# Kernel tuning notes

Hardware: AMD Instinct MI355X
Metric: run time of the kernel (lower is better)

## Reference

```python
import jax, jax.numpy as jnp
import numpy as np

S = 7          # grid size
C = 10         # num classes (SVHN digits)
L_COORD = 5.0
L_NOOBJ = 0.5
EPS = 1e-6     # safe-sqrt epsilon (original sqrt(clamp(x,0,1)) has inf grad at 0)


def _iou(b1, b2):
    """Vectorized translation of computeIOU. b1, b2: [..., 4] as (left, top, w, h)."""
    l1l, l1t, w1, h1 = b1[..., 0], b1[..., 1], b1[..., 2], b1[..., 3]
    l2l, l2t, w2, h2 = b2[..., 0], b2[..., 1], b2[..., 2], b2[..., 3]
    l1r, l1b = l1l + w1, l1t + h1
    l2r, l2b = l2l + w2, l2t + h2
    a1 = w1 * h1
    a2 = w2 * h2
    cont_by2 = (l2l <= l1l) & (l2t <= l1t) & (l2r >= l1r) & (l2b >= l1b)  # box2 contains box1
    cont_by1 = (l1l <= l2l) & (l1t <= l2t) & (l1r >= l2r) & (l1b >= l2b)  # box1 contains box2
    sep = (l1r <= l2l) | (l2r <= l1l) | (l1b <= l2t) | (l2b <= l1t)       # disjoint
    iw = jnp.minimum(l1r, l2r) - jnp.maximum(l1l, l2l)
    ih = jnp.minimum(l1b, l2b) - jnp.maximum(l1t, l2t)
    inter = iw * ih
    gen = inter / (a1 + a2 - inter)
    return jnp.where(cont_by2, a1 / a2,
           jnp.where(cont_by1, a2 / a1,
           jnp.where(sep, jnp.zeros_like(gen), gen)))


def setup_inputs() -> dict:
    key = jax.random.key(0)
    k1, k2, k3, k4 = jax.random.split(key, 4)
    N = 16384
    pred_tensor = jax.random.normal(k1, (N, S, S, 20), dtype=jnp.float32)
    xywh = jax.random.uniform(k2, (N, S, S, 4), dtype=jnp.float32)
    conf = (jax.random.uniform(k3, (N, S, S, 1)) < 0.15).astype(jnp.float32)  # ~7 objects/img
    cls = jax.random.randint(k4, (N, S, S, 1), 0, C).astype(jnp.float32)
    target_tensor = jnp.concatenate([xywh, conf, cls], axis=-1)
    return {"pred_tensor": pred_tensor, "target_tensor": target_tensor}


def reference(pred_tensor, target_tensor):
    N = pred_tensor.shape[0]
    conf_t = target_tensor[..., 4]                       # [N,S,S]
    coo = (conf_t > 0).astype(pred_tensor.dtype)
    noo = (conf_t == 0).astype(pred_tensor.dtype)

    # no-object confidence loss: both predicted confidences vs target conf (=0 on noo cells)
    noobj_loss = jnp.sum(noo * ((pred_tensor[..., 4] - conf_t) ** 2 +
                                (pred_tensor[..., 9] - conf_t) ** 2))

    # responsible-box selection via IoU (vectorized replacement of the python loop)
    bt = target_tensor[..., :4]                          # target box [N,S,S,4]
    bp0 = pred_tensor[..., 0:5]
    bp1 = pred_tensor[..., 5:10]
    iou0 = _iou(bp0[..., :4], bt)
    iou1 = _iou(bp1[..., :4], bt)
    pick0 = iou0 >= iou1                                 # box0 responsible when tie or higher
    max_iou = jax.lax.stop_gradient(jnp.where(pick0, iou0, iou1))  # Variable() detach in orig
    resp = jnp.where(pick0[..., None], bp0, bp1)         # responsible pred box [N,S,S,5]
    nonresp = jnp.where(pick0[..., None], bp1, bp0)

    contain_loss = jnp.sum(coo * (resp[..., 4] - max_iou) ** 2)

    xy_p = jnp.clip(resp[..., :2], 0.0, 1.0)
    xy_t = jnp.clip(bt[..., :2], 0.0, 1.0)
    wh_p = jnp.sqrt(jnp.clip(resp[..., 2:4], EPS, 1.0))
    wh_t = jnp.sqrt(jnp.clip(bt[..., 2:4], EPS, 1.0))
    loc_loss = jnp.sum(coo[..., None] * ((xy_p - xy_t) ** 2 + (wh_p - wh_t) ** 2))

    not_contain_loss = jnp.sum(coo * nonresp[..., 4] ** 2)  # target conf forced to 0

    # class cross-entropy (sum reduction) over object cells
    logits = pred_tensor[..., 10:]                       # [N,S,S,10]
    logz = jax.nn.logsumexp(logits, axis=-1)
    cls_idx = target_tensor[..., 5].astype(jnp.int32)
    picked = jnp.take_along_axis(logits, cls_idx[..., None], axis=-1)[..., 0]
    class_loss = jnp.sum(coo * (logz - picked))

    total = (L_COORD * loc_loss + 2.0 * contain_loss + not_contain_loss +
             L_NOOBJ * noobj_loss + class_loss)
    return total / N
```

## Files before the change

### kernel.cpp

```cpp
#include <hip/hip_runtime.h>
#include <hip/hip_bf16.h>


#define SBLK 256

constexpr float L_COORD = 5.0f;
constexpr float L_NOOBJ = 0.5f;
constexpr float EPS_    = 1e-6f;

__device__ __forceinline__ float iou_f(float l1l, float l1t, float w1, float h1,
                                       float l2l, float l2t, float w2, float h2) {
    float l1r = l1l + w1, l1b = l1t + h1;
    float l2r = l2l + w2, l2b = l2t + h2;
    float a1 = w1 * h1, a2 = w2 * h2;
    bool cont_by2 = (l2l <= l1l) && (l2t <= l1t) && (l2r >= l1r) && (l2b >= l1b);
    bool cont_by1 = (l1l <= l2l) && (l1t <= l2t) && (l1r >= l2r) && (l1b >= l2b);
    bool sep = (l1r <= l2l) || (l2r <= l1l) || (l1b <= l2t) || (l2b <= l1t);
    float iw = fminf(l1r, l2r) - fmaxf(l1l, l2l);
    float ih = fminf(l1b, l2b) - fmaxf(l1t, l2t);
    float inter = iw * ih;
    float gen = inter / (a1 + a2 - inter);
    float r = sep ? 0.0f : gen;
    r = cont_by1 ? (a2 / a1) : r;
    r = cont_by2 ? (a1 / a2) : r;
    return r;
}

__device__ __forceinline__ float clamp01(float x) { return fminf(fmaxf(x, 0.0f), 1.0f); }

__global__ __launch_bounds__(SBLK) void yolo_loss_kernel(
        const float* __restrict__ pred, const float* __restrict__ tgt,
        double* __restrict__ partials, int ncells) {
    int i = blockIdx.x * SBLK + threadIdx.x;
    float total = 0.0f;
    if (i < ncells) {
        const float4* p4 = reinterpret_cast<const float4*>(pred + (size_t)i * 20);
        float4 pa = p4[0];
        float4 pb = p4[1];
        float4 pc = p4[2];
        float4 pd = p4[3];
        float4 pe = p4[4];
        const float2* t2 = reinterpret_cast<const float2*>(tgt + (size_t)i * 6);
        float2 t0 = t2[0];
        float2 t1 = t2[1];
        float2 tc = t2[2];

        float conf = tc.x;
        float coo = (conf > 0.0f) ? 1.0f : 0.0f;
        float noo = (conf == 0.0f) ? 1.0f : 0.0f;

        float d0 = pb.x - conf, d1 = pc.y - conf;
        float noobj = noo * (d0 * d0 + d1 * d1);

        float b0l = pa.x, b0t = pa.y, b0w = pa.z, b0h = pa.w, b0c = pb.x;
        float b1l = pb.y, b1t = pb.z, b1w = pb.w, b1h = pc.x, b1c = pc.y;
        float btl = t0.x, btt = t0.y, btw = t1.x, bth = t1.y;

        float iou0 = iou_f(b0l, b0t, b0w, b0h, btl, btt, btw, bth);
        float iou1 = iou_f(b1l, b1t, b1w, b1h, btl, btt, btw, bth);
        bool pick0 = (iou0 >= iou1);
        float max_iou = pick0 ? iou0 : iou1;

        float rl = pick0 ? b0l : b1l;
        float rt = pick0 ? b0t : b1t;
        float rw = pick0 ? b0w : b1w;
        float rh = pick0 ? b0h : b1h;
        float rc = pick0 ? b0c : b1c;
        float nc = pick0 ? b1c : b0c;

        float cd = rc - max_iou;
        float contain = cd * cd;
        float not_contain = nc * nc;

        float ex = clamp01(rl) - clamp01(btl);
        float ey = clamp01(rt) - clamp01(btt);
        float sw = sqrtf(fminf(fmaxf(rw, EPS_), 1.0f)) - sqrtf(fminf(fmaxf(btw, EPS_), 1.0f));
        float sh = sqrtf(fminf(fmaxf(rh, EPS_), 1.0f)) - sqrtf(fminf(fmaxf(bth, EPS_), 1.0f));
        float loc = ex * ex + ey * ey + sw * sw + sh * sh;

        float lg0 = pc.z, lg1 = pc.w;
        float lg2 = pd.x, lg3 = pd.y, lg4 = pd.z, lg5 = pd.w;
        float lg6 = pe.x, lg7 = pe.y, lg8 = pe.z, lg9 = pe.w;
        float m = fmaxf(lg0, lg1);
        m = fmaxf(m, fmaxf(lg2, lg3));
        m = fmaxf(m, fmaxf(lg4, lg5));
        m = fmaxf(m, fmaxf(lg6, lg7));
        m = fmaxf(m, fmaxf(lg8, lg9));
        float ssum = __expf(lg0 - m) + __expf(lg1 - m) + __expf(lg2 - m) +
                     __expf(lg3 - m) + __expf(lg4 - m) + __expf(lg5 - m) +
                     __expf(lg6 - m) + __expf(lg7 - m) + __expf(lg8 - m) +
                     __expf(lg9 - m);
        float logz = m + __logf(ssum);
        int ci = (int)tc.y;
        float picked = lg0;
        picked = (ci == 1) ? lg1 : picked;
        picked = (ci == 2) ? lg2 : picked;
        picked = (ci == 3) ? lg3 : picked;
        picked = (ci == 4) ? lg4 : picked;
        picked = (ci == 5) ? lg5 : picked;
        picked = (ci == 6) ? lg6 : picked;
        picked = (ci == 7) ? lg7 : picked;
        picked = (ci == 8) ? lg8 : picked;
        picked = (ci == 9) ? lg9 : picked;
        float cls_loss = logz - picked;

        total = L_COORD * (coo * loc)
              + 2.0f * (coo * contain)
              + (coo * not_contain)
              + L_NOOBJ * noobj
              + coo * cls_loss;
    }

    double v = (double)total;
    #pragma unroll
    for (int off = 32; off > 0; off >>= 1)
        v += __shfl_down(v, off, 64);
    __shared__ double sm[SBLK / 64];
    int lane = threadIdx.x & 63;
    int wid  = threadIdx.x >> 6;
    if (lane == 0) sm[wid] = v;
    __syncthreads();
    if (threadIdx.x == 0) {
        double s = 0.0;
        #pragma unroll
        for (int w = 0; w < SBLK / 64; ++w) s += sm[w];
        partials[blockIdx.x] = s;
    }
}

#define RBLK 1024

__global__ __launch_bounds__(RBLK) void yolo_reduce_kernel(
        const double* __restrict__ partials, int nparts,
        float* __restrict__ out, double invN) {
    double v = 0.0;
    for (int idx = threadIdx.x; idx < nparts; idx += RBLK)
        v += partials[idx];
    #pragma unroll
    for (int off = 32; off > 0; off >>= 1)
        v += __shfl_down(v, off, 64);
    __shared__ double sm[RBLK / 64];
    int lane = threadIdx.x & 63;
    int wid  = threadIdx.x >> 6;
    if (lane == 0) sm[wid] = v;
    __syncthreads();
    if (threadIdx.x == 0) {
        double s = 0.0;
        #pragma unroll
        for (int w = 0; w < RBLK / 64; ++w) s += sm[w];
        out[0] = (float)(s * invN);
    }
}

extern "C" void kernel_launch(void* const* d_in, const int* in_sizes, int n_in,
                              void* d_out, int out_size, void* d_ws, size_t ws_size,
                              hipStream_t stream) {
    const float* pred = (const float*)d_in[0];
    const float* tgt  = (const float*)d_in[1];
    int ncells = in_sizes[0] / 20;
    int N = ncells / 49;

    int nblocks = (ncells + SBLK - 1) / SBLK;
    yolo_loss_kernel<<<nblocks, SBLK, 0, stream>>>(pred, tgt, (double*)d_ws, ncells);
    yolo_reduce_kernel<<<1, RBLK, 0, stream>>>((const double*)d_ws, nblocks,
                                               (float*)d_out, 1.0 / (double)N);
}
```

Before: 21.79 us.

## Stage pred loads through LDS via global_load_lds and use fast math intrinsics

Each block now loads its contiguous pred slab into shared memory with coalesced direct global-to-LDS 16-byte transfers, replacing per-thread strided float4 loads. Threads then read their five float4 values from LDS after a barrier. Divisions and sqrt switch to hardware rcp/sqrt intrinsics, and the intra-block reduction runs in float instead of double. This adds a barrier and 20KB of LDS per block, which may lower occupancy, and slightly reduces precision.

```diff
diff --git a/kernel.cpp b/kernel.cpp
--- a/kernel.cpp
+++ b/kernel.cpp
@@ -1,5 +1,4 @@
 #include <hip/hip_runtime.h>
-#include <hip/hip_bf16.h>
 
 
 #define SBLK 256
@@ -7,6 +6,11 @@
 constexpr float L_COORD = 5.0f;
 constexpr float L_NOOBJ = 0.5f;
 constexpr float EPS_    = 1e-6f;
+
+typedef __attribute__((address_space(3))) uint32_t lds_u32_t;
+typedef const __attribute__((address_space(1))) uint32_t glb_u32_t;
+
+__device__ __forceinline__ float clamp01(float x) { return fminf(fmaxf(x, 0.0f), 1.0f); }
 
 __device__ __forceinline__ float iou_f(float l1l, float l1t, float w1, float h1,
                                        float l2l, float l2t, float w2, float h2) {
@@ -19,31 +23,47 @@
     float iw = fminf(l1r, l2r) - fmaxf(l1l, l2l);
     float ih = fminf(l1b, l2b) - fmaxf(l1t, l2t);
     float inter = iw * ih;
-    float gen = inter / (a1 + a2 - inter);
+    float gen = inter * __builtin_amdgcn_rcpf(a1 + a2 - inter);
     float r = sep ? 0.0f : gen;
-    r = cont_by1 ? (a2 / a1) : r;
-    r = cont_by2 ? (a1 / a2) : r;
+    r = cont_by1 ? a2 * __builtin_amdgcn_rcpf(a1) : r;
+    r = cont_by2 ? a1 * __builtin_amdgcn_rcpf(a2) : r;
     return r;
 }
-
-__device__ __forceinline__ float clamp01(float x) { return fminf(fmaxf(x, 0.0f), 1.0f); }
 
 __global__ __launch_bounds__(SBLK) void yolo_loss_kernel(
         const float* __restrict__ pred, const float* __restrict__ tgt,
         double* __restrict__ partials, int ncells) {
-    int i = blockIdx.x * SBLK + threadIdx.x;
+    __shared__ float4 sp4[SBLK * 5];
+    int block0 = blockIdx.x * SBLK;
+    int i = block0 + threadIdx.x;
+
+    const float4* pg = reinterpret_cast<const float4*>(pred) + (size_t)block0 * 5;
+    int nf4 = (ncells - block0) * 5;
+    #pragma unroll
+    for (int k = 0; k < 5; ++k) {
+        int j = threadIdx.x + k * SBLK;
+        if (j < nf4) {
+            __builtin_amdgcn_global_load_lds((glb_u32_t*)(pg + j),
+                                             (lds_u32_t*)(&sp4[j]), 16, 0, 0);
+        }
+    }
+
+    float2 t0, t1, tc;
+    if (i < ncells) {
+        const float2* tg = reinterpret_cast<const float2*>(tgt) + (size_t)i * 3;
+        t0 = tg[0]; t1 = tg[1]; tc = tg[2];
+    } else {
+        t0 = t1 = tc = make_float2(0.f, 0.f);
+    }
+    __syncthreads();
+
     float total = 0.0f;
     if (i < ncells) {
-        const float4* p4 = reinterpret_cast<const float4*>(pred + (size_t)i * 20);
-        float4 pa = p4[0];
-        float4 pb = p4[1];
-        float4 pc = p4[2];
-        float4 pd = p4[3];
-        float4 pe = p4[4];
-        const float2* t2 = reinterpret_cast<const float2*>(tgt + (size_t)i * 6);
-        float2 t0 = t2[0];
-        float2 t1 = t2[1];
-        float2 tc = t2[2];
+        float4 pa = sp4[threadIdx.x * 5 + 0];
+        float4 pb = sp4[threadIdx.x * 5 + 1];
+        float4 pc = sp4[threadIdx.x * 5 + 2];
+        float4 pd = sp4[threadIdx.x * 5 + 3];
+        float4 pe = sp4[threadIdx.x * 5 + 4];
 
         float conf = tc.x;
         float coo = (conf > 0.0f) ? 1.0f : 0.0f;
@@ -74,8 +94,10 @@
 
         float ex = clamp01(rl) - clamp01(btl);
         float ey = clamp01(rt) - clamp01(btt);
-        float sw = sqrtf(fminf(fmaxf(rw, EPS_), 1.0f)) - sqrtf(fminf(fmaxf(btw, EPS_), 1.0f));
-        float sh = sqrtf(fminf(fmaxf(rh, EPS_), 1.0f)) - sqrtf(fminf(fmaxf(bth, EPS_), 1.0f));
+        float sw = __builtin_amdgcn_sqrtf(fminf(fmaxf(rw, EPS_), 1.0f))
+                 - __builtin_amdgcn_sqrtf(fminf(fmaxf(btw, EPS_), 1.0f));
+        float sh = __builtin_amdgcn_sqrtf(fminf(fmaxf(rh, EPS_), 1.0f))
+                 - __builtin_amdgcn_sqrtf(fminf(fmaxf(bth, EPS_), 1.0f));
         float loc = ex * ex + ey * ey + sw * sw + sh * sh;
 
         float lg0 = pc.z, lg1 = pc.w;
@@ -111,19 +133,19 @@
               + coo * cls_loss;
     }
 
-    double v = (double)total;
+    float v = total;
     #pragma unroll
     for (int off = 32; off > 0; off >>= 1)
         v += __shfl_down(v, off, 64);
-    __shared__ double sm[SBLK / 64];
+    __shared__ float smw[SBLK / 64];
     int lane = threadIdx.x & 63;
     int wid  = threadIdx.x >> 6;
-    if (lane == 0) sm[wid] = v;
+    if (lane == 0) smw[wid] = v;
     __syncthreads();
     if (threadIdx.x == 0) {
         double s = 0.0;
         #pragma unroll
-        for (int w = 0; w < SBLK / 64; ++w) s += sm[w];
+        for (int w = 0; w < SBLK / 64; ++w) s += (double)smw[w];
         partials[blockIdx.x] = s;
     }
 }
```

After: 22.20 us. No clear change (+1.9%).
